# Kernel tuning notes

Measured on AMD Instinct MI355X. Metric: run time of the kernel, lower is better.

Reference implementation:

```python
import math
import jax, jax.numpy as jnp
import numpy as np

DIM = 1024
HID = 2048  # int(dim * expansion_factor)
QK = 128
G = 256     # group size
B, N = 4, 4096
NUM_BUCKETS = 32
MAX_DIST = 128


def _rel_pos_bias(rel_emb, g, scale):
    # non-causal T5 relative position bucket (num_buckets halved to 16)
    pos = jnp.arange(g)
    rel = pos[None, :] - pos[:, None]          # k_pos - q_pos
    n = -rel
    nb = NUM_BUCKETS // 2                       # 16
    ret = (n < 0).astype(jnp.int32) * nb
    n = jnp.abs(n)
    max_exact = nb // 2                         # 8
    is_small = n < max_exact
    val_large = max_exact + (
        jnp.log(jnp.maximum(n, 1).astype(jnp.float32) / max_exact)
        / math.log(MAX_DIST / max_exact) * (nb - max_exact)
    ).astype(jnp.int32)
    val_large = jnp.minimum(val_large, nb - 1)
    bucket = ret + jnp.where(is_small, n, val_large)   # [g, g] in [0, 32)
    return rel_emb[bucket, 0] * scale                   # [g, g]


def _layernorm(x, g, b, eps=1e-5):
    mu = jnp.mean(x, axis=-1, keepdims=True)
    var = jnp.mean((x - mu) ** 2, axis=-1, keepdims=True)
    return (x - mu) * jax.lax.rsqrt(var + eps) * g + b


def setup_inputs() -> dict:
    key = jax.random.key(0)
    ks = jax.random.split(key, 8)
    return {
        "x": jax.random.normal(ks[0], (B, N, DIM), dtype=jnp.float32),
        "ln_g": jnp.ones((DIM,), jnp.float32),
        "ln_b": jnp.zeros((DIM,), jnp.float32),
        "W_h": jax.random.normal(ks[1], (DIM, 2 * HID), jnp.float32) * 0.02,
        "b_h": jnp.zeros((2 * HID,), jnp.float32),
        "W_qk": jax.random.normal(ks[2], (DIM, QK), jnp.float32) * 0.02,
        "b_qk": jnp.zeros((QK,), jnp.float32),
        "os_gamma": jax.random.normal(ks[3], (4, QK), jnp.float32) * 0.02,
        "os_beta": jnp.zeros((4, QK), jnp.float32),
        "rel_emb": jax.random.normal(ks[4], (NUM_BUCKETS, 1), jnp.float32) * 0.02,
        "W_out": jax.random.normal(ks[5], (HID, DIM), jnp.float32) * 0.02,
        "b_out": jnp.zeros((DIM,), jnp.float32),
    }


def reference(x, ln_g, ln_b, W_h, b_h, W_qk, b_qk, os_gamma, os_beta, rel_emb, W_out, b_out):
    b, n = x.shape[0], x.shape[1]
    ng = n // G
    normed = _layernorm(x, ln_g, ln_b)
    hid = jax.nn.silu(normed @ W_h + b_h)               # [b, n, 2*HID]
    v, gate = hid[..., :HID], hid[..., HID:]
    qk = jax.nn.silu(normed @ W_qk + b_qk)              # [b, n, QK]
    # OffsetScale heads=4 -> quad_q, lin_q, quad_k, lin_k
    heads = qk[..., None, :] * os_gamma + os_beta        # [b, n, 4, QK]
    quad_q, lin_q, quad_k, lin_k = [heads[..., h, :] for h in range(4)]
    # group into blocks of G
    def grp(t):
        return t.reshape(b, ng, G, t.shape[-1])
    quad_q, quad_k, lin_q, lin_k, vg = map(grp, (quad_q, quad_k, lin_q, lin_k, v))
    # quadratic (local) branch: ReLU^2 attention per group + T5 bias
    sim = jnp.einsum('bgid,bgjd->bgij', quad_q, quad_k) / G
    sim = sim + _rel_pos_bias(rel_emb, G, QK ** 0.5)
    attn = jax.nn.relu(sim) ** 2
    quad_out = jnp.einsum('bgij,bgje->bgie', attn, vg)   # [b, ng, G, HID]
    # linear (global) branch, reduced over groups (non-causal)
    lin_kv = jnp.einsum('bgnd,bgne->bde', lin_k, vg) / n
    lin_out = jnp.einsum('bde,bgnd->bgne', lin_kv, lin_q)
    out = (quad_out + lin_out).reshape(b, n, HID)
    out = gate * out
    return out @ W_out + b_out + x
```

## Files before the change

kernel.cpp:

```cpp
#include <hip/hip_runtime.h>
#include <hip/hip_bf16.h>


typedef __attribute__((ext_vector_type(8))) short short8;
typedef __attribute__((ext_vector_type(4))) float f32x4;

#define BM 128
#define BN 128
#define BK 32

struct Aux {
  const float* b1;
  const float* x;
  const float* gamma;
  const float* beta;
  const float* biastab;
  const unsigned short* a2;
  const unsigned short* bkv;
  const unsigned short* gate;
  unsigned short* o16a;
  unsigned short* o16b;
  unsigned short* o16c;
  unsigned short* o16d;
  float* o32;
};

__device__ __forceinline__ float bf2f(unsigned short u) {
  union { float f; unsigned int i; } w; w.i = ((unsigned int)u) << 16; return w.f;
}
__device__ __forceinline__ unsigned short f2bf(float f) {
  union { float f; unsigned int i; } w; w.f = f;
  unsigned int x = w.i;
  return (unsigned short)((x + 0x7FFFu + ((x >> 16) & 1u)) >> 16);
}
__device__ __forceinline__ float silu_f(float z) { return z / (1.0f + __expf(-z)); }

__device__ __forceinline__ void async_cp16(const void* g, void* l) {
  __builtin_amdgcn_global_load_lds(
      (const __attribute__((address_space(1))) void*)g,
      (__attribute__((address_space(3))) void*)l, 16, 0, 0);
}

__device__ __forceinline__ float block_sum(float v) {
  #pragma unroll
  for (int o = 32; o > 0; o >>= 1) v += __shfl_down(v, o, 64);
  __shared__ float sh[4];
  __syncthreads();
  if ((threadIdx.x & 63) == 0) sh[threadIdx.x >> 6] = v;
  __syncthreads();
  return sh[0] + sh[1] + sh[2] + sh[3];
}

__global__ __launch_bounds__(256) void ln_k(const float* __restrict__ x,
                                            const float* __restrict__ g,
                                            const float* __restrict__ b,
                                            unsigned short* __restrict__ out) {
  const int row = blockIdx.x;
  const int tid = threadIdx.x;
  const float4 xv = ((const float4*)(x + (size_t)row * 1024))[tid];
  float s = xv.x + xv.y + xv.z + xv.w;
  s = block_sum(s);
  const float mu = s * (1.0f / 1024.0f);
  const float d0 = xv.x - mu, d1 = xv.y - mu, d2 = xv.z - mu, d3 = xv.w - mu;
  float q = d0 * d0 + d1 * d1 + d2 * d2 + d3 * d3;
  q = block_sum(q);
  const float rstd = rsqrtf(q * (1.0f / 1024.0f) + 1e-5f);
  const float4 gv = ((const float4*)g)[tid];
  const float4 bv = ((const float4*)b)[tid];
  unsigned short* o = out + (size_t)row * 1024 + tid * 4;
  o[0] = f2bf(d0 * rstd * gv.x + bv.x);
  o[1] = f2bf(d1 * rstd * gv.y + bv.y);
  o[2] = f2bf(d2 * rstd * gv.z + bv.z);
  o[3] = f2bf(d3 * rstd * gv.w + bv.w);
}

__global__ __launch_bounds__(256) void tc_k(const float* __restrict__ in,
                                            unsigned short* __restrict__ out,
                                            int K, int N) {
  __shared__ unsigned short L[64][65];
  const int t = threadIdx.x;
  const int k0 = blockIdx.y * 64, n0 = blockIdx.x * 64;
  const int r = t >> 4, c4 = (t & 15) * 4;
  #pragma unroll
  for (int rr = 0; rr < 4; ++rr) {
    const int kk = rr * 16 + r;
    const float4 f = ((const float4*)(in + (size_t)(k0 + kk) * N + n0))[t & 15];
    L[kk][c4 + 0] = f2bf(f.x); L[kk][c4 + 1] = f2bf(f.y);
    L[kk][c4 + 2] = f2bf(f.z); L[kk][c4 + 3] = f2bf(f.w);
  }
  __syncthreads();
  #pragma unroll
  for (int rr = 0; rr < 4; ++rr) {
    const int nn = rr * 16 + r;
    ushort4 u;
    u.x = L[c4 + 0][nn]; u.y = L[c4 + 1][nn];
    u.z = L[c4 + 2][nn]; u.w = L[c4 + 3][nn];
    ((ushort4*)(out + (size_t)(n0 + nn) * K + k0))[t & 15] = u;
  }
}

__global__ void bias_k(const float* __restrict__ rel, float* __restrict__ tab) {
  int idx = blockIdx.x * 256 + threadIdx.x;
  if (idx >= 511) return;
  int d = idx - 255;
  int n = -d;
  int ret = (n < 0) ? 16 : 0;
  int a = (n < 0) ? -n : n;
  int bucket;
  if (a < 8) {
    bucket = ret + a;
  } else {
    float t = __logf((float)a * 0.125f) / 2.7725887298583984f * 8.0f;
    int vl = 8 + (int)t;
    if (vl > 15) vl = 15;
    bucket = ret + vl;
  }
  tab[idx] = rel[bucket] * 11.313708498984761f;
}

__global__ void kvred_k(const float* __restrict__ pkv, unsigned short* __restrict__ linkvT) {
  int i4 = blockIdx.x * 256 + threadIdx.x;
  const int b = i4 >> 16, rem = i4 & 65535;
  const float4* p = (const float4*)(pkv + (size_t)b * 1048576) + rem;
  const float4 p0 = p[0], p1 = p[65536], p2 = p[131072], p3 = p[196608];
  ushort4 u;
  u.x = f2bf((p0.x + p1.x + p2.x + p3.x) * (1.0f / 4096.0f));
  u.y = f2bf((p0.y + p1.y + p2.y + p3.y) * (1.0f / 4096.0f));
  u.z = f2bf((p0.z + p1.z + p2.z + p3.z) * (1.0f / 4096.0f));
  u.w = f2bf((p0.w + p1.w + p2.w + p3.w) * (1.0f / 4096.0f));
  ((ushort4*)(linkvT + (size_t)b * 262144))[rem] = u;
}

template<int MODE>
__global__ __launch_bounds__(512, 2) void gemm256_k(
    const unsigned short* __restrict__ Ag,
    const unsigned short* __restrict__ Bg,
    int lda, int ldb, int kiters, Aux aux)
{
  extern __shared__ __align__(16) char smem[];

  const int tid  = threadIdx.x;
  const int lane = tid & 63;
  const int wave = tid >> 6;
  const int quad = lane >> 4;
  const int l16  = lane & 15;
  const int wm   = (wave >> 2) * 128;
  const int wn   = (wave & 3) * 64;

  const int L  = blockIdx.x + gridDim.x * blockIdx.y;
  const int p  = L & 7;
  const int s  = L >> 3;
  const int bx = s >> 3;
  const int by = p * 8 + (s & 7);
  const int bm = by * 256;
  const int bn = bx * 256;

  const size_t lda2 = (size_t)lda * 2;
  const size_t ldb2 = (size_t)ldb * 2;

  const int srow  = tid >> 2;
  const int scolb = ((tid & 3) ^ ((tid >> 3) & 3)) << 4;
  const char* gA = (const char*)Ag + (size_t)(bm + srow) * lda2 + scolb;
  const char* gB = (const char*)Bg + (size_t)(bn + srow) * ldb2 + scolb;
  char* laBase = smem + wave * 1024;

  auto stage = [&](int tt) {
    char* la = laBase + (tt & 3) * 32768;
    const char* a = gA + (size_t)tt * 64;
    const char* b = gB + (size_t)tt * 64;
    async_cp16(a,              la);
    async_cp16(a + 128 * lda2, la + 8192);
    async_cp16(b,              la + 16384);
    async_cp16(b + 128 * ldb2, la + 24576);
  };

  const f32x4 zero = {0.f, 0.f, 0.f, 0.f};
  f32x4 acc[8][4];
  #pragma unroll
  for (int i = 0; i < 8; ++i)
    #pragma unroll
    for (int j = 0; j < 4; ++j) acc[i][j] = zero;

  stage(0); stage(1); stage(2);

  const int cw = (quad ^ ((l16 >> 1) & 3)) << 4;
  const char* rdA = smem + (wm + l16) * 64 + cw;
  const char* rdB = smem + 16384 + (wn + l16) * 64 + cw;

  short8 fA[12], fB[12];

  asm volatile("s_waitcnt vmcnt(8)" ::: "memory");
  asm volatile("s_barrier" ::: "memory");
  #pragma unroll
  for (int i = 0; i < 8; ++i) fA[i]     = *(const short8*)(rdA + i * 1024);
  #pragma unroll
  for (int j = 0; j < 4; ++j) fA[8 + j] = *(const short8*)(rdB + j * 1024);

#define TILE_BODY(T, CUR, NXT)                                                 \
  do {                                                                         \
    const int t_ = (T);                                                        \
    if (t_ + 1 < kiters) {                                                     \
      if (t_ + 2 < kiters) asm volatile("s_waitcnt vmcnt(4)" ::: "memory");    \
      else                 asm volatile("s_waitcnt vmcnt(0)" ::: "memory");    \
    }                                                                          \
    asm volatile("s_barrier" ::: "memory");                                    \
    if (t_ + 3 < kiters) stage(t_ + 3);                                        \
    if (t_ + 1 < kiters) {                                                     \
      const unsigned s1 = (unsigned)((t_ + 1) & 3) * 32768u;                   \
      _Pragma("unroll")                                                        \
      for (int i = 0; i < 8; ++i)                                              \
        NXT[i]     = *(const short8*)(rdA + s1 + i * 1024);                    \
      _Pragma("unroll")                                                        \
      for (int j = 0; j < 4; ++j)                                              \
        NXT[8 + j] = *(const short8*)(rdB + s1 + j * 1024);                    \
    }                                                                          \
    __builtin_amdgcn_sched_barrier(0);                                         \
    __builtin_amdgcn_s_setprio(1);                                             \
    _Pragma("unroll")                                                          \
    for (int i = 0; i < 8; ++i)                                                \
      _Pragma("unroll")                                                        \
      for (int j = 0; j < 4; ++j)                                              \
        acc[i][j] = __builtin_amdgcn_mfma_f32_16x16x32_bf16(                   \
            CUR[i], CUR[8 + j], acc[i][j], 0, 0, 0);                           \
    __builtin_amdgcn_s_setprio(0);                                             \
    __builtin_amdgcn_sched_barrier(0);                                         \
  } while (0)

  for (int t = 0; t < kiters; t += 2) {
    TILE_BODY(t,     fA, fB);
    TILE_BODY(t + 1, fB, fA);
  }
#undef TILE_BODY

  #pragma unroll
  for (int i = 0; i < 8; ++i) {
    #pragma unroll
    for (int j = 0; j < 4; ++j) {
      const int row0 = bm + wm + i * 16 + quad * 4;
      const int col  = bn + wn + j * 16 + l16;
      if constexpr (MODE == 0) {
        const float bb = aux.b1[col];
        float s4[4];
        #pragma unroll
        for (int r = 0; r < 4; ++r) s4[r] = silu_f(acc[i][j][r] + bb);
        if (bn < 2048) {
          const int b = row0 >> 12, tt = row0 & 4095;
          ushort4 u; u.x = f2bf(s4[0]); u.y = f2bf(s4[1]); u.z = f2bf(s4[2]); u.w = f2bf(s4[3]);
          *(ushort4*)(aux.o16a + (size_t)b * 8388608 + (size_t)col * 4096 + tt) = u;
        } else {
          #pragma unroll
          for (int r = 0; r < 4; ++r)
            aux.o16b[(size_t)(row0 + r) * 2048 + (col - 2048)] = f2bf(s4[r]);
        }
      } else {
        #pragma unroll
        for (int r = 0; r < 4; ++r) {
          const size_t idx = (size_t)(row0 + r) * 1024 + col;
          aux.o32[idx] = acc[i][j][r] + aux.b1[col] + aux.x[idx];
        }
      }
    }
  }
}

template<int MODE>
__global__ __launch_bounds__(256, 2) void gemm_k(
    const unsigned short* __restrict__ Ag,
    const unsigned short* __restrict__ Bg,
    int lda, int ldb, int kiters, Aux aux)
{
  __shared__ unsigned short As[BM * BK];
  __shared__ unsigned short Bs[BN * BK];

  const int tid  = threadIdx.x;
  const int lane = tid & 63;
  const int wave = tid >> 6;
  const int quad = lane >> 4;
  const int l16  = lane & 15;
  const int wm   = (wave >> 1) * 64;
  const int wn   = (wave & 1) * 64;
  const int bz   = blockIdx.z;
  const int bm   = blockIdx.y * BM;
  const int bn   = blockIdx.x * BN;

  const unsigned short* A = Ag;
  const unsigned short* B = Bg;
  if constexpr (MODE == 2) { A += (size_t)bz * 32768;  B += (size_t)bz * 32768; }
  if constexpr (MODE == 3) { A += (size_t)bz * 65536;
                             B += (size_t)(bz >> 4) * 8388608 + (size_t)(bz & 15) * 256; }
  if constexpr (MODE == 4) { const int b = bz >> 2, s = bz & 3;
                             A += (size_t)b * 524288 + (size_t)s * 1024;
                             B += (size_t)b * 8388608 + (size_t)s * 1024; }

  const unsigned short* A2 = nullptr;
  const unsigned short* B2 = nullptr;
  if constexpr (MODE == 3) {
    A2 = aux.a2 + (size_t)bz * 32768;
    B2 = aux.bkv + (size_t)(bz >> 4) * 262144;
  }

  const int srow = wave * 32 + (lane >> 2);
  const int scol = (lane & 3) * 8;
  unsigned short* lA = As + wave * 1024;
  unsigned short* lB = Bs + wave * 1024;

  const f32x4 zero = {0.f, 0.f, 0.f, 0.f};
  f32x4 acc[4][4];
  #pragma unroll
  for (int i = 0; i < 4; ++i)
    #pragma unroll
    for (int j = 0; j < 4; ++j) acc[i][j] = zero;

  for (int kt = 0; kt < kiters; ++kt) {
    const unsigned short* pa = A;
    const unsigned short* pb = B;
    int la = lda, lb = ldb, kk = kt * BK;
    if constexpr (MODE == 3) {
      if (kt >= 8) { pa = A2; pb = B2; la = 128; lb = 128; kk -= 256; }
    }

    __syncthreads();
    async_cp16(pa + (size_t)(bm + srow) * la + kk + scol, lA);
    async_cp16(pa + (size_t)(bm + srow + 16) * la + kk + scol, lA + 512);
    async_cp16(pb + (size_t)(bn + srow) * lb + kk + scol, lB);
    async_cp16(pb + (size_t)(bn + srow + 16) * lb + kk + scol, lB + 512);
    __syncthreads();

    short8 af[4], bfv[4];
    #pragma unroll
    for (int i = 0; i < 4; ++i)
      af[i] = *reinterpret_cast<const short8*>(As + (wm + i * 16 + l16) * BK + quad * 8);
    #pragma unroll
    for (int j = 0; j < 4; ++j)
      bfv[j] = *reinterpret_cast<const short8*>(Bs + (wn + j * 16 + l16) * BK + quad * 8);

    #pragma unroll
    for (int i = 0; i < 4; ++i)
      #pragma unroll
      for (int j = 0; j < 4; ++j)
        acc[i][j] = __builtin_amdgcn_mfma_f32_16x16x32_bf16(af[i], bfv[j], acc[i][j], 0, 0, 0);
  }

  #pragma unroll
  for (int i = 0; i < 4; ++i) {
    #pragma unroll
    for (int j = 0; j < 4; ++j) {
      const int row0 = bm + wm + i * 16 + quad * 4;
      const int col  = bn + wn + j * 16 + l16;
      if constexpr (MODE == 1) {
        const float bb = aux.b1[col];
        float s[4];
        #pragma unroll
        for (int r = 0; r < 4; ++r) s[r] = silu_f(acc[i][j][r] + bb);
        #pragma unroll
        for (int r = 0; r < 4; ++r) {
          const size_t idx = (size_t)(row0 + r) * 128 + col;
          aux.o16a[idx] = f2bf(s[r] * aux.gamma[col]       + aux.beta[col]);
          aux.o16b[idx] = f2bf(s[r] * aux.gamma[128 + col] + aux.beta[128 + col]);
          aux.o16c[idx] = f2bf(s[r] * aux.gamma[256 + col] + aux.beta[256 + col]);
        }
        const int b = row0 >> 12, t = row0 & 4095;
        const float g4 = aux.gamma[384 + col], b4 = aux.beta[384 + col];
        ushort4 u;
        u.x = f2bf(s[0] * g4 + b4); u.y = f2bf(s[1] * g4 + b4);
        u.z = f2bf(s[2] * g4 + b4); u.w = f2bf(s[3] * g4 + b4);
        *(ushort4*)(aux.o16d + (size_t)b * 524288 + (size_t)col * 4096 + t) = u;
      } else if constexpr (MODE == 2) {
        #pragma unroll
        for (int r = 0; r < 4; ++r) {
          float s = acc[i][j][r] * (1.0f / 256.0f) + aux.biastab[col - (row0 + r) + 255];
          s = fmaxf(s, 0.0f);
          aux.o16a[(size_t)bz * 65536 + (size_t)(row0 + r) * 256 + col] = f2bf(s * s);
        }
      } else if constexpr (MODE == 3) {
        #pragma unroll
        for (int r = 0; r < 4; ++r) {
          const size_t idx = ((size_t)bz * 256 + row0 + r) * 2048 + col;
          aux.o16a[idx] = f2bf(acc[i][j][r] * bf2f(aux.gate[idx]));
        }
      } else if constexpr (MODE == 4) {
        float4 u; u.x = acc[i][j][0]; u.y = acc[i][j][1]; u.z = acc[i][j][2]; u.w = acc[i][j][3];
        *(float4*)(aux.o32 + (size_t)bz * 262144 + (size_t)col * 128 + row0) = u;
      }
    }
  }
}

extern "C" void kernel_launch(void* const* d_in, const int* in_sizes, int n_in,
                              void* d_out, int out_size, void* d_ws, size_t ws_size,
                              hipStream_t stream) {
  (void)in_sizes; (void)n_in; (void)out_size; (void)ws_size;
  const float* x     = (const float*)d_in[0];
  const float* ln_g  = (const float*)d_in[1];
  const float* ln_b  = (const float*)d_in[2];
  const float* W_h   = (const float*)d_in[3];
  const float* b_h   = (const float*)d_in[4];
  const float* W_qk  = (const float*)d_in[5];
  const float* b_qk  = (const float*)d_in[6];
  const float* osg   = (const float*)d_in[7];
  const float* osb   = (const float*)d_in[8];
  const float* rel   = (const float*)d_in[9];
  const float* W_out = (const float*)d_in[10];
  const float* b_out = (const float*)d_in[11];
  float* out = (float*)d_out;

  static bool attr_done = false;
  if (!attr_done) {
    hipFuncSetAttribute(reinterpret_cast<const void*>(gemm256_k<0>),
                        hipFuncAttributeMaxDynamicSharedMemorySize, 131072);
    hipFuncSetAttribute(reinterpret_cast<const void*>(gemm256_k<6>),
                        hipFuncAttributeMaxDynamicSharedMemorySize, 131072);
    attr_done = true;
  }

  char* w = (char*)d_ws;
  size_t off = 0;
  auto alloc = [&](size_t bytes) { char* p = w + off; off += (bytes + 255) & ~(size_t)255; return p; };

  unsigned short* normed = (unsigned short*)alloc(16384ull * 1024 * 2);
  unsigned short* whT    = (unsigned short*)alloc(4096ull * 1024 * 2);
  unsigned short* qq     = (unsigned short*)alloc(16384ull * 128 * 2);
  unsigned short* qkk    = (unsigned short*)alloc(16384ull * 128 * 2);
  unsigned short* linkT  = (unsigned short*)alloc(4ull * 128 * 4096 * 2);
  float*          pkvT   = (float*)alloc(16ull * 2048 * 128 * 4);
  unsigned short* wqkT   = (unsigned short*)alloc(128ull * 1024 * 2);
  unsigned short* woutT  = (unsigned short*)alloc(1024ull * 2048 * 2);
  unsigned short* vT     = (unsigned short*)alloc(4ull * 2048 * 4096 * 2);
  unsigned short* gate   = (unsigned short*)alloc(16384ull * 2048 * 2);
  unsigned short* lq     = (unsigned short*)alloc(16384ull * 128 * 2);
  unsigned short* attn   = (unsigned short*)alloc(64ull * 256 * 256 * 2);
  unsigned short* linkvT = (unsigned short*)alloc(4ull * 2048 * 128 * 2);
  float*          btab   = (float*)alloc(511 * 4);
  unsigned short* gated  = (unsigned short*)w;

  tc_k<<<dim3(64, 16), 256, 0, stream>>>(W_h,   whT,   1024, 4096);
  tc_k<<<dim3(2, 16),  256, 0, stream>>>(W_qk,  wqkT,  1024, 128);
  tc_k<<<dim3(16, 32), 256, 0, stream>>>(W_out, woutT, 2048, 1024);
  bias_k<<<2, 256, 0, stream>>>(rel, btab);
  ln_k<<<16384, 256, 0, stream>>>(x, ln_g, ln_b, normed);

  Aux a0{}; a0.b1 = b_h; a0.o16a = vT; a0.o16b = gate;
  gemm256_k<0><<<dim3(16, 64), 512, 131072, stream>>>(normed, whT, 1024, 1024, 32, a0);

  Aux a1{}; a1.b1 = b_qk; a1.gamma = osg; a1.beta = osb;
  a1.o16a = qq; a1.o16b = lq; a1.o16c = qkk; a1.o16d = linkT;
  gemm_k<1><<<dim3(1, 128, 1), 256, 0, stream>>>(normed, wqkT, 1024, 1024, 32, a1);

  Aux a2x{}; a2x.biastab = btab; a2x.o16a = attn;
  gemm_k<2><<<dim3(2, 2, 64), 256, 0, stream>>>(qq, qkk, 128, 128, 4, a2x);

  Aux a4{}; a4.o32 = pkvT;
  gemm_k<4><<<dim3(16, 1, 16), 256, 0, stream>>>(linkT, vT, 4096, 4096, 8, a4);

  kvred_k<<<1024, 256, 0, stream>>>(pkvT, linkvT);

  Aux a3{}; a3.a2 = lq; a3.bkv = linkvT; a3.gate = gate; a3.o16a = gated;
  gemm_k<3><<<dim3(16, 2, 64), 256, 0, stream>>>(attn, vT, 256, 4096, 12, a3);

  Aux a6{}; a6.b1 = b_out; a6.x = x; a6.o32 = out;
  gemm256_k<6><<<dim3(4, 64), 512, 131072, stream>>>(gated, woutT, 2048, 2048, 64, a6);
}
```

Measured before the change: 573.7 us.

## Move attention-output GEMM to 256x256 pipelined kernel and merge prep kernels

The attention-times-V plus linear-branch GEMM (mode 3) moves from the 128x128 single-buffered kernel to the 256x256, 512-thread kernel with a 4-stage async copy pipeline. That kernel now handles the two-source K loop (attn/vT, then lin_q/lin_kv) and the gated epilogue. Separately, the three weight-transpose launches and the bias-table launch are merged into one prep kernel to cut launch overhead. The larger tiles should improve data reuse and latency hiding, but the grid shrinks to 512 blocks, which may lower occupancy.

New measurement: 608.9 us. 1.06x slower.

```diff
diff --git a/kernel.cpp b/kernel.cpp
--- a/kernel.cpp
+++ b/kernel.cpp
@@ -74,12 +74,12 @@
   o[3] = f2bf(d3 * rstd * gv.w + bv.w);
 }
 
-__global__ __launch_bounds__(256) void tc_k(const float* __restrict__ in,
-                                            unsigned short* __restrict__ out,
-                                            int K, int N) {
+__device__ __forceinline__ void tc_body(const float* __restrict__ in,
+                                        unsigned short* __restrict__ out,
+                                        int K, int N, int bx, int by) {
   __shared__ unsigned short L[64][65];
   const int t = threadIdx.x;
-  const int k0 = blockIdx.y * 64, n0 = blockIdx.x * 64;
+  const int k0 = by * 64, n0 = bx * 64;
   const int r = t >> 4, c4 = (t & 15) * 4;
   #pragma unroll
   for (int rr = 0; rr < 4; ++rr) {
@@ -99,23 +99,41 @@
   }
 }
 
-__global__ void bias_k(const float* __restrict__ rel, float* __restrict__ tab) {
-  int idx = blockIdx.x * 256 + threadIdx.x;
-  if (idx >= 511) return;
-  int d = idx - 255;
-  int n = -d;
-  int ret = (n < 0) ? 16 : 0;
-  int a = (n < 0) ? -n : n;
-  int bucket;
-  if (a < 8) {
-    bucket = ret + a;
+__global__ __launch_bounds__(256) void prep_k(const float* __restrict__ W_h,
+                                              const float* __restrict__ W_qk,
+                                              const float* __restrict__ W_out,
+                                              const float* __restrict__ rel,
+                                              unsigned short* __restrict__ whT,
+                                              unsigned short* __restrict__ wqkT,
+                                              unsigned short* __restrict__ woutT,
+                                              float* __restrict__ tab) {
+  const int b = blockIdx.x;
+  if (b < 1024) {
+    tc_body(W_h, whT, 1024, 4096, b & 63, b >> 6);
+  } else if (b < 1056) {
+    const int c = b - 1024;
+    tc_body(W_qk, wqkT, 1024, 128, c & 1, c >> 1);
+  } else if (b < 1568) {
+    const int c = b - 1056;
+    tc_body(W_out, woutT, 2048, 1024, c & 15, c >> 4);
   } else {
-    float t = __logf((float)a * 0.125f) / 2.7725887298583984f * 8.0f;
-    int vl = 8 + (int)t;
-    if (vl > 15) vl = 15;
-    bucket = ret + vl;
-  }
-  tab[idx] = rel[bucket] * 11.313708498984761f;
+    int idx = (b - 1568) * 256 + threadIdx.x;
+    if (idx >= 511) return;
+    int d = idx - 255;
+    int n = -d;
+    int ret = (n < 0) ? 16 : 0;
+    int a = (n < 0) ? -n : n;
+    int bucket;
+    if (a < 8) {
+      bucket = ret + a;
+    } else {
+      float t = __logf((float)a * 0.125f) / 2.7725887298583984f * 8.0f;
+      int vl = 8 + (int)t;
+      if (vl > 15) vl = 15;
+      bucket = ret + vl;
+    }
+    tab[idx] = rel[bucket] * 11.313708498984761f;
+  }
 }
 
 __global__ void kvred_k(const float* __restrict__ pkv, unsigned short* __restrict__ linkvT) {
@@ -147,31 +165,54 @@
   const int wm   = (wave >> 2) * 128;
   const int wn   = (wave & 3) * 64;
 
-  const int L  = blockIdx.x + gridDim.x * blockIdx.y;
-  const int p  = L & 7;
-  const int s  = L >> 3;
-  const int bx = s >> 3;
-  const int by = p * 8 + (s & 7);
-  const int bm = by * 256;
-  const int bn = bx * 256;
+  int bm, bn, g = 0;
+  if constexpr (MODE == 3) {
+    g  = blockIdx.y;
+    bm = 0;
+    bn = blockIdx.x * 256;
+  } else {
+    const int L  = blockIdx.x + gridDim.x * blockIdx.y;
+    const int p  = L & 7;
+    const int s  = L >> 3;
+    bm = (p * 8 + (s & 7)) * 256;
+    bn = (s >> 3) * 256;
+  }
 
   const size_t lda2 = (size_t)lda * 2;
   const size_t ldb2 = (size_t)ldb * 2;
 
   const int srow  = tid >> 2;
   const int scolb = ((tid & 3) ^ ((tid >> 3) & 3)) << 4;
-  const char* gA = (const char*)Ag + (size_t)(bm + srow) * lda2 + scolb;
-  const char* gB = (const char*)Bg + (size_t)(bn + srow) * ldb2 + scolb;
+  const char *gA, *gB, *gA2 = nullptr, *gB2 = nullptr;
+  if constexpr (MODE == 3) {
+    gA  = (const char*)Ag + (size_t)g * 131072 + (size_t)srow * 512 + scolb;
+    gA2 = (const char*)aux.a2 + (size_t)g * 65536 + (size_t)srow * 256 + scolb;
+    gB  = (const char*)Bg + (size_t)(g >> 4) * 16777216 + (size_t)(g & 15) * 512
+          + (size_t)(bn + srow) * 8192 + scolb;
+    gB2 = (const char*)aux.bkv + (size_t)(g >> 4) * 524288
+          + (size_t)(bn + srow) * 256 + scolb;
+  } else {
+    gA = (const char*)Ag + (size_t)(bm + srow) * lda2 + scolb;
+    gB = (const char*)Bg + (size_t)(bn + srow) * ldb2 + scolb;
+  }
   char* laBase = smem + wave * 1024;
 
   auto stage = [&](int tt) {
     char* la = laBase + (tt & 3) * 32768;
-    const char* a = gA + (size_t)tt * 64;
-    const char* b = gB + (size_t)tt * 64;
-    async_cp16(a,              la);
-    async_cp16(a + 128 * lda2, la + 8192);
-    async_cp16(b,              la + 16384);
-    async_cp16(b + 128 * ldb2, la + 24576);
+    const char *a, *b; size_t sA, sB;
+    if constexpr (MODE == 3) {
+      if (tt >= 8) { a = gA2 + (size_t)(tt - 8) * 64; sA = 256;
+                     b = gB2 + (size_t)(tt - 8) * 64; sB = 256; }
+      else         { a = gA  + (size_t)tt * 64;       sA = 512;
+                     b = gB  + (size_t)tt * 64;       sB = 8192; }
+    } else {
+      a = gA + (size_t)tt * 64; sA = lda2;
+      b = gB + (size_t)tt * 64; sB = ldb2;
+    }
+    async_cp16(a,            la);
+    async_cp16(a + 128 * sA, la + 8192);
+    async_cp16(b,            la + 16384);
+    async_cp16(b + 128 * sB, la + 24576);
   };
 
   const f32x4 zero = {0.f, 0.f, 0.f, 0.f};
@@ -252,6 +293,12 @@
           for (int r = 0; r < 4; ++r)
             aux.o16b[(size_t)(row0 + r) * 2048 + (col - 2048)] = f2bf(s4[r]);
         }
+      } else if constexpr (MODE == 3) {
+        #pragma unroll
+        for (int r = 0; r < 4; ++r) {
+          const size_t idx = ((size_t)g * 256 + row0 + r) * 2048 + col;
+          aux.o16a[idx] = f2bf(acc[i][j][r] * bf2f(aux.gate[idx]));
+        }
       } else {
         #pragma unroll
         for (int r = 0; r < 4; ++r) {
@@ -286,18 +333,9 @@
   const unsigned short* A = Ag;
   const unsigned short* B = Bg;
   if constexpr (MODE == 2) { A += (size_t)bz * 32768;  B += (size_t)bz * 32768; }
-  if constexpr (MODE == 3) { A += (size_t)bz * 65536;
-                             B += (size_t)(bz >> 4) * 8388608 + (size_t)(bz & 15) * 256; }
   if constexpr (MODE == 4) { const int b = bz >> 2, s = bz & 3;
                              A += (size_t)b * 524288 + (size_t)s * 1024;
                              B += (size_t)b * 8388608 + (size_t)s * 1024; }
-
-  const unsigned short* A2 = nullptr;
-  const unsigned short* B2 = nullptr;
-  if constexpr (MODE == 3) {
-    A2 = aux.a2 + (size_t)bz * 32768;
-    B2 = aux.bkv + (size_t)(bz >> 4) * 262144;
-  }
 
   const int srow = wave * 32 + (lane >> 2);
   const int scol = (lane & 3) * 8;
@@ -312,18 +350,13 @@
     for (int j = 0; j < 4; ++j) acc[i][j] = zero;
 
   for (int kt = 0; kt < kiters; ++kt) {
-    const unsigned short* pa = A;
-    const unsigned short* pb = B;
-    int la = lda, lb = ldb, kk = kt * BK;
-    if constexpr (MODE == 3) {
-      if (kt >= 8) { pa = A2; pb = B2; la = 128; lb = 128; kk -= 256; }
-    }
+    const int kk = kt * BK;
 
     __syncthreads();
-    async_cp16(pa + (size_t)(bm + srow) * la + kk + scol, lA);
-    async_cp16(pa + (size_t)(bm + srow + 16) * la + kk + scol, lA + 512);
-    async_cp16(pb + (size_t)(bn + srow) * lb + kk + scol, lB);
-    async_cp16(pb + (size_t)(bn + srow + 16) * lb + kk + scol, lB + 512);
+    async_cp16(A + (size_t)(bm + srow) * lda + kk + scol, lA);
+    async_cp16(A + (size_t)(bm + srow + 16) * lda + kk + scol, lA + 512);
+    async_cp16(B + (size_t)(bn + srow) * ldb + kk + scol, lB);
+    async_cp16(B + (size_t)(bn + srow + 16) * ldb + kk + scol, lB + 512);
     __syncthreads();
 
     short8 af[4], bfv[4];
@@ -371,12 +404,6 @@
           float s = acc[i][j][r] * (1.0f / 256.0f) + aux.biastab[col - (row0 + r) + 255];
           s = fmaxf(s, 0.0f);
           aux.o16a[(size_t)bz * 65536 + (size_t)(row0 + r) * 256 + col] = f2bf(s * s);
-        }
-      } else if constexpr (MODE == 3) {
-        #pragma unroll
-        for (int r = 0; r < 4; ++r) {
-          const size_t idx = ((size_t)bz * 256 + row0 + r) * 2048 + col;
-          aux.o16a[idx] = f2bf(acc[i][j][r] * bf2f(aux.gate[idx]));
         }
       } else if constexpr (MODE == 4) {
         float4 u; u.x = acc[i][j][0]; u.y = acc[i][j][1]; u.z = acc[i][j][2]; u.w = acc[i][j][3];
@@ -408,6 +435,8 @@
   if (!attr_done) {
     hipFuncSetAttribute(reinterpret_cast<const void*>(gemm256_k<0>),
                         hipFuncAttributeMaxDynamicSharedMemorySize, 131072);
+    hipFuncSetAttribute(reinterpret_cast<const void*>(gemm256_k<3>),
+                        hipFuncAttributeMaxDynamicSharedMemorySize, 131072);
     hipFuncSetAttribute(reinterpret_cast<const void*>(gemm256_k<6>),
                         hipFuncAttributeMaxDynamicSharedMemorySize, 131072);
     attr_done = true;
@@ -433,10 +462,7 @@
   float*          btab   = (float*)alloc(511 * 4);
   unsigned short* gated  = (unsigned short*)w;
 
-  tc_k<<<dim3(64, 16), 256, 0, stream>>>(W_h,   whT,   1024, 4096);
-  tc_k<<<dim3(2, 16),  256, 0, stream>>>(W_qk,  wqkT,  1024, 128);
-  tc_k<<<dim3(16, 32), 256, 0, stream>>>(W_out, woutT, 2048, 1024);
-  bias_k<<<2, 256, 0, stream>>>(rel, btab);
+  prep_k<<<1570, 256, 0, stream>>>(W_h, W_qk, W_out, rel, whT, wqkT, woutT, btab);
   ln_k<<<16384, 256, 0, stream>>>(x, ln_g, ln_b, normed);
 
   Aux a0{}; a0.b1 = b_h; a0.o16a = vT; a0.o16b = gate;
@@ -455,7 +481,7 @@
   kvred_k<<<1024, 256, 0, stream>>>(pkvT, linkvT);
 
   Aux a3{}; a3.a2 = lq; a3.bkv = linkvT; a3.gate = gate; a3.o16a = gated;
-  gemm_k<3><<<dim3(16, 2, 64), 256, 0, stream>>>(attn, vT, 256, 4096, 12, a3);
+  gemm256_k<3><<<dim3(8, 64), 512, 131072, stream>>>(attn, vT, 256, 4096, 12, a3);
 
   Aux a6{}; a6.b1 = b_out; a6.x = x; a6.o32 = out;
   gemm256_k<6><<<dim3(4, 64), 512, 131072, stream>>>(gated, woutT, 2048, 2048, 64, a6);
```
